# Optimization experiments

Hardware: AMD Instinct MI355X
Metric: run time of the kernel (lower is better)

The kernel has to match this reference:

```python
import jax, jax.numpy as jnp
import numpy as np

EPS = 0.0001
N, E, DIN, H, DH, C, G = 50000, 800000, 256, 4, 64, 10, 100


def setup_inputs() -> dict:
    key = jax.random.key(0)
    ks = jax.random.split(key, 10)
    x = jax.random.normal(ks[0], (N, DIN), dtype=jnp.float32)
    src = jax.random.randint(ks[1], (E,), 0, N)
    dst = jax.random.randint(ks[2], (E,), 0, N)
    midx = jnp.stack([src, dst]).astype(jnp.int32)
    batch = jnp.sort(jax.random.randint(ks[3], (N,), 0, G)).astype(jnp.int32)
    W_feat = jax.random.normal(ks[4], (DIN, H * DH), dtype=jnp.float32) / np.sqrt(DIN)
    phi = jax.random.normal(ks[5], (H, 2 * DH, 1), dtype=jnp.float32) / np.sqrt(2 * DH)
    W1 = jax.random.normal(ks[6], (H * DH, DH), dtype=jnp.float32) / np.sqrt(H * DH)
    b1 = jnp.zeros((DH,), jnp.float32)
    W2 = jax.random.normal(ks[7], (DH, C), dtype=jnp.float32) / np.sqrt(DH)
    b2 = jnp.zeros((C,), jnp.float32)
    return {"x": x, "midx": midx, "batch": batch, "W_feat": W_feat,
            "phi": phi, "W1": W1, "b1": b1, "W2": W2, "b2": b2}


def reference(x, midx, batch, W_feat, phi, W1, b1, W2, b2):
    src, dst = midx[0], midx[1]
    # per-head node features [N, H, DH]
    h = (x @ W_feat).reshape(-1, H, DH)
    # concat-then-matmul with phi == sum of two half projections (GAT trick)
    phi_s = phi[:, :DH, 0]   # [H, DH]
    phi_d = phi[:, DH:, 0]   # [H, DH]
    a_s = jnp.einsum('nhd,hd->nh', h, phi_s)  # [N, H]
    a_d = jnp.einsum('nhd,hd->nh', h, phi_d)
    w = jax.nn.sigmoid(jax.nn.leaky_relu(a_s[src] + a_d[dst]))  # [E, H]
    msg = (h[dst] * w[:, :, None]).reshape(src.shape[0], H * DH)  # [E, H*DH]
    agg = jax.ops.segment_sum(msg, src, num_segments=x.shape[0])  # scatter_add
    # MLP head (dropout is identity in eval mode)
    z = jax.nn.leaky_relu(agg @ W1 + b1) @ W2 + b2  # [N, C]
    tmp = jnp.exp(z - jnp.max(z, axis=-1, keepdims=True)) + EPS
    preds = tmp / jnp.sum(tmp, axis=-1, keepdims=True)
    # global mean pool over graphs
    sums = jax.ops.segment_sum(preds, batch, num_segments=G)
    cnts = jax.ops.segment_sum(jnp.ones((batch.shape[0],), preds.dtype), batch, num_segments=G)
    yp = sums / cnts[:, None]
    return jnp.log(yp), preds
```

## Files before the change

kernel.cpp:

```cpp
#include <hip/hip_runtime.h>
#include <hip/hip_bf16.h>
#include <cstdint>

#define NN   50000
#define EE   800000
#define DIN_ 256
#define HD_  256
#define DH_  64
#define NH_  4
#define NC_  10
#define NG_  100
#define EPS_ 1e-4f
#define SLOPE_ 0.01f
#define AROW 40
#define CAP_ 48

typedef unsigned short ushortT;
typedef __attribute__((ext_vector_type(8))) short short8;
typedef __attribute__((ext_vector_type(4))) float f32x4;

__device__ __forceinline__ float leaky(float x) { return x >= 0.f ? x : SLOPE_ * x; }
__device__ __forceinline__ float sigm(float x)  { return 1.f / (1.f + __expf(-x)); }
__device__ __forceinline__ float b2f(ushortT u) { return __uint_as_float(((unsigned)u) << 16); }
__device__ __forceinline__ ushortT f2b(float f) {
    unsigned u = __float_as_uint(f);
    u += 0x7fffu + ((u >> 16) & 1u);
    return (ushortT)(u >> 16);
}

__global__ void setup_kernel(int* cursor,
                             const float* __restrict__ W, ushortT* __restrict__ wt,
                             const float* __restrict__ W1, ushortT* __restrict__ w1t,
                             const int* __restrict__ batch, int* __restrict__ gstart) {
    int i = blockIdx.x * 256 + threadIdx.x;
    if (i < NN) {
        cursor[i] = 0;
        int b = batch[i];
        int bp = (i == 0) ? -1 : batch[i - 1];
        for (int g = bp + 1; g <= b; g++) gstart[g] = i;
        if (i == NN - 1) {
            for (int g = b + 1; g <= NG_; g++) gstart[g] = NN;
        }
    }
    if (i < DIN_ * HD_) {
        int k = i >> 8, n = i & 255;
        wt[n * DIN_ + k] = f2b(W[i]);
    }
    if (i < 256 * 64) {
        int k = i >> 6, o = i & 63;
        w1t[o * 256 + k] = f2b(W1[i]);
    }
}

__global__ __launch_bounds__(256) void gemm_attn(const float* __restrict__ x,
                                                 const ushortT* __restrict__ wt,
                                                 const float* __restrict__ phi,
                                                 ushortT* __restrict__ hbf,
                                                 float* __restrict__ a_s,
                                                 float* __restrict__ a_d) {
    __shared__ ushortT A_lds[128 * AROW];
    __shared__ ushortT B_lds[128 * AROW];
    const int tid  = threadIdx.x;
    const int wave = tid >> 6, lane = tid & 63;
    const int wm = wave >> 1, wn = wave & 1;
    const int row0 = blockIdx.x * 128;
    const int col0 = blockIdx.y * 128;
    const int q = lane >> 4, l16 = lane & 15;

    f32x4 acc[4][4];
#pragma unroll
    for (int i = 0; i < 4; i++)
#pragma unroll
        for (int j = 0; j < 4; j++) acc[i][j] = (f32x4){0.f, 0.f, 0.f, 0.f};

    const int lm  = tid >> 1;
    const int lko = (tid & 1) * 16;

    for (int k0 = 0; k0 < DIN_; k0 += 32) {
        __syncthreads();
        {
            int gr = row0 + lm;
            float4 a0 = make_float4(0.f,0.f,0.f,0.f), a1 = a0, a2 = a0, a3 = a0;
            if (gr < NN) {
                const float4* xp = (const float4*)(x + (size_t)gr * DIN_ + k0 + lko);
                a0 = xp[0]; a1 = xp[1]; a2 = xp[2]; a3 = xp[3];
            }
            ushortT* ap = &A_lds[lm * AROW + lko];
            *(ushort4*)(ap + 0)  = make_ushort4(f2b(a0.x), f2b(a0.y), f2b(a0.z), f2b(a0.w));
            *(ushort4*)(ap + 4)  = make_ushort4(f2b(a1.x), f2b(a1.y), f2b(a1.z), f2b(a1.w));
            *(ushort4*)(ap + 8)  = make_ushort4(f2b(a2.x), f2b(a2.y), f2b(a2.z), f2b(a2.w));
            *(ushort4*)(ap + 12) = make_ushort4(f2b(a3.x), f2b(a3.y), f2b(a3.z), f2b(a3.w));
        }
        {
            const uint4* wp = (const uint4*)(wt + (size_t)(col0 + lm) * DIN_ + k0 + lko);
            uint4 b0 = wp[0], b1 = wp[1];
            *(uint4*)&B_lds[lm * AROW + lko + 0] = b0;
            *(uint4*)&B_lds[lm * AROW + lko + 8] = b1;
        }
        __syncthreads();

        short8 af[4], bf[4];
#pragma unroll
        for (int mi = 0; mi < 4; mi++)
            af[mi] = *(const short8*)&A_lds[(wm * 64 + mi * 16 + l16) * AROW + q * 8];
#pragma unroll
        for (int ni = 0; ni < 4; ni++)
            bf[ni] = *(const short8*)&B_lds[(wn * 64 + ni * 16 + l16) * AROW + q * 8];
#pragma unroll
        for (int mi = 0; mi < 4; mi++)
#pragma unroll
            for (int ni = 0; ni < 4; ni++)
                acc[mi][ni] = __builtin_amdgcn_mfma_f32_16x16x32_bf16(af[mi], bf[ni], acc[mi][ni], 0, 0, 0);
    }

#pragma unroll
    for (int mi = 0; mi < 4; mi++) {
        int rbase = row0 + wm * 64 + mi * 16 + q * 4;
#pragma unroll
        for (int ni = 0; ni < 4; ni++) {
            int c = col0 + wn * 64 + ni * 16 + l16;
#pragma unroll
            for (int r = 0; r < 4; r++) {
                int gr = rbase + r;
                if (gr < NN) hbf[(size_t)gr * HD_ + c] = f2b(acc[mi][ni][r]);
            }
        }
    }

    int head = blockIdx.y * 2 + wn;
    float phs[4], phd[4];
#pragma unroll
    for (int ni = 0; ni < 4; ni++) {
        phs[ni] = phi[head * 128 + ni * 16 + l16];
        phd[ni] = phi[head * 128 + 64 + ni * 16 + l16];
    }
#pragma unroll
    for (int mi = 0; mi < 4; mi++) {
#pragma unroll
        for (int r = 0; r < 4; r++) {
            float ps = acc[mi][0][r] * phs[0] + acc[mi][1][r] * phs[1]
                     + acc[mi][2][r] * phs[2] + acc[mi][3][r] * phs[3];
            float pd = acc[mi][0][r] * phd[0] + acc[mi][1][r] * phd[1]
                     + acc[mi][2][r] * phd[2] + acc[mi][3][r] * phd[3];
#pragma unroll
            for (int o = 1; o < 16; o <<= 1) {
                ps += __shfl_xor(ps, o);
                pd += __shfl_xor(pd, o);
            }
            if (l16 == 0) {
                int gr = row0 + wm * 64 + mi * 16 + q * 4 + r;
                if (gr < NN) {
                    a_s[gr * 4 + head] = ps;
                    a_d[gr * 4 + head] = pd;
                }
            }
        }
    }
}

__global__ void fill_edges(const int* __restrict__ src, const int* __restrict__ dstA,
                           int* __restrict__ cursor,
                           const float* __restrict__ a_s, const float* __restrict__ a_d,
                           uint4* __restrict__ edges) {
    int e = blockIdx.x * 256 + threadIdx.x;
    if (e >= EE) return;
    int s = src[e], d = dstA[e];
    int slot = atomicAdd(&cursor[s], 1);
    if (slot >= CAP_) return;
    float4 as4 = *(const float4*)(a_s + (size_t)s * 4);
    float4 ad4 = *(const float4*)(a_d + (size_t)d * 4);
    unsigned w01 = (unsigned)f2b(sigm(leaky(as4.x + ad4.x)))
                 | ((unsigned)f2b(sigm(leaky(as4.y + ad4.y))) << 16);
    unsigned w23 = (unsigned)f2b(sigm(leaky(as4.z + ad4.z)))
                 | ((unsigned)f2b(sigm(leaky(as4.w + ad4.w))) << 16);
    edges[(size_t)s * CAP_ + slot] = make_uint4((unsigned)d, w01, w23, 0u);
}

__global__ __launch_bounds__(256) void agg_kernel(const ushortT* __restrict__ hbf,
                                                  const int* __restrict__ cursor,
                                                  const uint4* __restrict__ edges,
                                                  ushortT* __restrict__ aggB) {
    int wv = threadIdx.x >> 6, lane = threadIdx.x & 63;
    int n = blockIdx.x * 4 + wv;
    int hsel = lane >> 4;
    int wsh = (hsel & 1) * 16;
    int cnt = cursor[n];
    if (cnt > CAP_) cnt = CAP_;
    int e0 = n * CAP_, e1 = e0 + cnt;
    float4 acc = make_float4(0.f, 0.f, 0.f, 0.f);
    const ushortT* hbase = hbf + (size_t)lane * 4;

    int i = e0;
    while (i + 8 <= e1) {
        uint4 ee[8]; ushort4 hh[8]; float ww[8];
#pragma unroll
        for (int j = 0; j < 8; j++) ee[j] = edges[i + j];
#pragma unroll
        for (int j = 0; j < 8; j++) {
            unsigned pair = (hsel & 2) ? ee[j].z : ee[j].y;
            ww[j] = b2f((ushortT)((pair >> wsh) & 0xffffu));
            hh[j] = *(const ushort4*)(hbase + (size_t)ee[j].x * HD_);
        }
#pragma unroll
        for (int j = 0; j < 8; j++) {
            acc.x += b2f(hh[j].x) * ww[j];
            acc.y += b2f(hh[j].y) * ww[j];
            acc.z += b2f(hh[j].z) * ww[j];
            acc.w += b2f(hh[j].w) * ww[j];
        }
        i += 8;
    }
    while (i + 4 <= e1) {
        uint4 ee[4]; ushort4 hh[4]; float ww[4];
#pragma unroll
        for (int j = 0; j < 4; j++) ee[j] = edges[i + j];
#pragma unroll
        for (int j = 0; j < 4; j++) {
            unsigned pair = (hsel & 2) ? ee[j].z : ee[j].y;
            ww[j] = b2f((ushortT)((pair >> wsh) & 0xffffu));
            hh[j] = *(const ushort4*)(hbase + (size_t)ee[j].x * HD_);
        }
#pragma unroll
        for (int j = 0; j < 4; j++) {
            acc.x += b2f(hh[j].x) * ww[j];
            acc.y += b2f(hh[j].y) * ww[j];
            acc.z += b2f(hh[j].z) * ww[j];
            acc.w += b2f(hh[j].w) * ww[j];
        }
        i += 4;
    }
    for (; i < e1; i++) {
        uint4 e = edges[i];
        unsigned pair = (hsel & 2) ? e.z : e.y;
        float s = b2f((ushortT)((pair >> wsh) & 0xffffu));
        ushort4 hv = *(const ushort4*)(hbase + (size_t)e.x * HD_);
        acc.x += b2f(hv.x) * s; acc.y += b2f(hv.y) * s;
        acc.z += b2f(hv.z) * s; acc.w += b2f(hv.w) * s;
    }
    ushort4 o4 = make_ushort4(f2b(acc.x), f2b(acc.y), f2b(acc.z), f2b(acc.w));
    *(ushort4*)(aggB + (size_t)n * HD_ + lane * 4) = o4;
}

__global__ __launch_bounds__(256) void mlp_kernel(const ushortT* __restrict__ aggB,
                                                  const ushortT* __restrict__ w1t,
                                                  const float* __restrict__ b1,
                                                  const float* __restrict__ W2,
                                                  const float* __restrict__ b2,
                                                  float* __restrict__ out) {
    __shared__ float z1t[64][65];
    const int tid = threadIdx.x;
    const int wave = tid >> 6, lane = tid & 63;
    const int q = lane >> 4, l16 = lane & 15;
    const int n0 = blockIdx.x * 64;
    const int nodeRow = n0 + wave * 16 + l16;

    f32x4 acc[4];
#pragma unroll
    for (int ni = 0; ni < 4; ni++) acc[ni] = (f32x4){0.f, 0.f, 0.f, 0.f};

    const ushortT* arow = aggB + (size_t)nodeRow * HD_ + q * 8;
#pragma unroll
    for (int k0 = 0; k0 < 256; k0 += 32) {
        short8 af = *(const short8*)(arow + k0);
#pragma unroll
        for (int ni = 0; ni < 4; ni++) {
            short8 bf = *(const short8*)(w1t + (size_t)(ni * 16 + l16) * 256 + k0 + q * 8);
            acc[ni] = __builtin_amdgcn_mfma_f32_16x16x32_bf16(af, bf, acc[ni], 0, 0, 0);
        }
    }
#pragma unroll
    for (int ni = 0; ni < 4; ni++) {
        int o = ni * 16 + l16;
        float bb = b1[o];
#pragma unroll
        for (int r = 0; r < 4; r++)
            z1t[o][wave * 16 + q * 4 + r] = leaky(acc[ni][r] + bb);
    }
    __syncthreads();

    if (tid < 64) {
        int n = n0 + tid;
        if (n < NN) {
            float zc[NC_];
#pragma unroll
            for (int c = 0; c < NC_; c++) zc[c] = b2[c];
            for (int k = 0; k < 64; k++) {
                float zv = z1t[k][tid];
#pragma unroll
                for (int c = 0; c < NC_; c++) zc[c] += zv * W2[k * NC_ + c];
            }
            float m = zc[0];
#pragma unroll
            for (int c = 1; c < NC_; c++) m = fmaxf(m, zc[c]);
            float ssum = 0.f;
#pragma unroll
            for (int c = 0; c < NC_; c++) { zc[c] = __expf(zc[c] - m) + EPS_; ssum += zc[c]; }
            float inv = 1.f / ssum;
#pragma unroll
            for (int c = 0; c < NC_; c++) out[1000 + (size_t)n * NC_ + c] = zc[c] * inv;
        }
    }
}

__global__ __launch_bounds__(256) void group_mean(const float* __restrict__ preds,
                                                  const int* __restrict__ gstart,
                                                  float* __restrict__ out) {
    __shared__ float red[16][16];
    int g = blockIdx.x;
    int t = threadIdx.x;
    int c = t & 15, chunk = t >> 4;
    int gs = gstart[g], ge = gstart[g + 1];
    float s = 0.f;
    if (c < NC_) {
        for (int n = gs + chunk; n < ge; n += 16) s += preds[(size_t)n * NC_ + c];
    }
    red[chunk][c] = s;
    __syncthreads();
    if (t < NC_) {
        float tot = 0.f;
#pragma unroll
        for (int j = 0; j < 16; j++) tot += red[j][t];
        out[g * NC_ + t] = __logf(tot / (float)(ge - gs));
    }
}

extern "C" void kernel_launch(void* const* d_in, const int* in_sizes, int n_in,
                              void* d_out, int out_size, void* d_ws, size_t ws_size,
                              hipStream_t stream) {
    const float* x      = (const float*)d_in[0];
    const int*   midx   = (const int*)d_in[1];
    const int*   batch  = (const int*)d_in[2];
    const float* W_feat = (const float*)d_in[3];
    const float* phi    = (const float*)d_in[4];
    const float* W1     = (const float*)d_in[5];
    const float* b1     = (const float*)d_in[6];
    const float* W2     = (const float*)d_in[7];
    const float* b2     = (const float*)d_in[8];
    const int* src = midx;
    const int* dst = midx + EE;
    float* out = (float*)d_out;

    char* p = (char*)d_ws;
    auto alloc = [&](size_t bytes) { void* r = (void*)p; p += (bytes + 255) & ~(size_t)255; return r; };
    ushortT* hbf      = (ushortT*)alloc((size_t)NN * HD_ * 2);
    ushortT* aggB     = (ushortT*)alloc((size_t)NN * HD_ * 2);
    uint4*   edges    = (uint4*)alloc((size_t)NN * CAP_ * 16);
    ushortT* wt       = (ushortT*)alloc((size_t)DIN_ * HD_ * 2);
    ushortT* w1t      = (ushortT*)alloc((size_t)64 * 256 * 2);
    float*   a_s      = (float*)alloc((size_t)NN * 4 * 4);
    float*   a_d      = (float*)alloc((size_t)NN * 4 * 4);
    int*     cursor   = (int*)alloc((size_t)NN * 4);
    int*     gstart   = (int*)alloc((size_t)(NG_ + 1) * 4);

    setup_kernel<<<256, 256, 0, stream>>>(cursor, W_feat, wt, W1, w1t, batch, gstart);
    gemm_attn<<<dim3((NN + 127) / 128, 2), 256, 0, stream>>>(x, wt, phi, hbf, a_s, a_d);
    fill_edges<<<(EE + 255) / 256, 256, 0, stream>>>(src, dst, cursor, a_s, a_d, edges);
    agg_kernel<<<NN / 4, 256, 0, stream>>>(hbf, cursor, edges, aggB);
    mlp_kernel<<<(NN + 63) / 64, 256, 0, stream>>>(aggB, w1t, b1, W2, b2, out);
    group_mean<<<NG_, 256, 0, stream>>>(out + 1000, gstart, out);
}
```

Baseline: 265.7 us.

## Fuse edge aggregation and MLP head into one kernel via LDS staging

Merges the aggregation kernel and the MLP kernel so each block aggregates 16 nodes into shared memory and immediately runs the W1 MFMA, the W2 projection and the softmax on them. This removes the global round trip of the 50000x256 bf16 aggregate buffer and one kernel launch. In exchange each block now processes 16 nodes with each wave doing four nodes sequentially, and only 16 threads run the tail MLP, so there is less parallelism per block and more serialized latency in the gather loop.

```diff
diff --git a/kernel.cpp b/kernel.cpp
--- a/kernel.cpp
+++ b/kernel.cpp
@@ -14,6 +14,7 @@
 #define SLOPE_ 0.01f
 #define AROW 40
 #define CAP_ 48
+#define FROW 264
 
 typedef unsigned short ushortT;
 typedef __attribute__((ext_vector_type(8))) short short8;
@@ -176,129 +177,124 @@
     edges[(size_t)s * CAP_ + slot] = make_uint4((unsigned)d, w01, w23, 0u);
 }
 
-__global__ __launch_bounds__(256) void agg_kernel(const ushortT* __restrict__ hbf,
-                                                  const int* __restrict__ cursor,
-                                                  const uint4* __restrict__ edges,
-                                                  ushortT* __restrict__ aggB) {
-    int wv = threadIdx.x >> 6, lane = threadIdx.x & 63;
-    int n = blockIdx.x * 4 + wv;
-    int hsel = lane >> 4;
-    int wsh = (hsel & 1) * 16;
-    int cnt = cursor[n];
-    if (cnt > CAP_) cnt = CAP_;
-    int e0 = n * CAP_, e1 = e0 + cnt;
-    float4 acc = make_float4(0.f, 0.f, 0.f, 0.f);
-    const ushortT* hbase = hbf + (size_t)lane * 4;
-
-    int i = e0;
-    while (i + 8 <= e1) {
-        uint4 ee[8]; ushort4 hh[8]; float ww[8];
-#pragma unroll
-        for (int j = 0; j < 8; j++) ee[j] = edges[i + j];
-#pragma unroll
-        for (int j = 0; j < 8; j++) {
-            unsigned pair = (hsel & 2) ? ee[j].z : ee[j].y;
-            ww[j] = b2f((ushortT)((pair >> wsh) & 0xffffu));
-            hh[j] = *(const ushort4*)(hbase + (size_t)ee[j].x * HD_);
-        }
-#pragma unroll
-        for (int j = 0; j < 8; j++) {
-            acc.x += b2f(hh[j].x) * ww[j];
-            acc.y += b2f(hh[j].y) * ww[j];
-            acc.z += b2f(hh[j].z) * ww[j];
-            acc.w += b2f(hh[j].w) * ww[j];
-        }
-        i += 8;
-    }
-    while (i + 4 <= e1) {
-        uint4 ee[4]; ushort4 hh[4]; float ww[4];
-#pragma unroll
-        for (int j = 0; j < 4; j++) ee[j] = edges[i + j];
-#pragma unroll
-        for (int j = 0; j < 4; j++) {
-            unsigned pair = (hsel & 2) ? ee[j].z : ee[j].y;
-            ww[j] = b2f((ushortT)((pair >> wsh) & 0xffffu));
-            hh[j] = *(const ushort4*)(hbase + (size_t)ee[j].x * HD_);
-        }
-#pragma unroll
-        for (int j = 0; j < 4; j++) {
-            acc.x += b2f(hh[j].x) * ww[j];
-            acc.y += b2f(hh[j].y) * ww[j];
-            acc.z += b2f(hh[j].z) * ww[j];
-            acc.w += b2f(hh[j].w) * ww[j];
-        }
-        i += 4;
-    }
-    for (; i < e1; i++) {
-        uint4 e = edges[i];
-        unsigned pair = (hsel & 2) ? e.z : e.y;
-        float s = b2f((ushortT)((pair >> wsh) & 0xffffu));
-        ushort4 hv = *(const ushort4*)(hbase + (size_t)e.x * HD_);
-        acc.x += b2f(hv.x) * s; acc.y += b2f(hv.y) * s;
-        acc.z += b2f(hv.z) * s; acc.w += b2f(hv.w) * s;
-    }
-    ushort4 o4 = make_ushort4(f2b(acc.x), f2b(acc.y), f2b(acc.z), f2b(acc.w));
-    *(ushort4*)(aggB + (size_t)n * HD_ + lane * 4) = o4;
-}
-
-__global__ __launch_bounds__(256) void mlp_kernel(const ushortT* __restrict__ aggB,
-                                                  const ushortT* __restrict__ w1t,
-                                                  const float* __restrict__ b1,
-                                                  const float* __restrict__ W2,
-                                                  const float* __restrict__ b2,
-                                                  float* __restrict__ out) {
-    __shared__ float z1t[64][65];
+__global__ __launch_bounds__(256) void agg_mlp(const ushortT* __restrict__ hbf,
+                                               const int* __restrict__ cursor,
+                                               const uint4* __restrict__ edges,
+                                               const ushortT* __restrict__ w1t,
+                                               const float* __restrict__ b1,
+                                               const float* __restrict__ W2,
+                                               const float* __restrict__ b2,
+                                               float* __restrict__ out) {
+    __shared__ ushortT A_lds[16 * FROW];
+    __shared__ float z1t[16][68];
     const int tid = threadIdx.x;
     const int wave = tid >> 6, lane = tid & 63;
     const int q = lane >> 4, l16 = lane & 15;
-    const int n0 = blockIdx.x * 64;
-    const int nodeRow = n0 + wave * 16 + l16;
-
-    f32x4 acc[4];
-#pragma unroll
-    for (int ni = 0; ni < 4; ni++) acc[ni] = (f32x4){0.f, 0.f, 0.f, 0.f};
-
-    const ushortT* arow = aggB + (size_t)nodeRow * HD_ + q * 8;
+    const int hsel = lane >> 4;
+    const int wsh = (hsel & 1) * 16;
+    const int n0 = blockIdx.x * 16;
+    const ushortT* hbase = hbf + (size_t)lane * 4;
+
+#pragma unroll
+    for (int ii = 0; ii < 4; ii++) {
+        int ln = wave * 4 + ii;
+        int n = n0 + ln;
+        int cnt = cursor[n];
+        if (cnt > CAP_) cnt = CAP_;
+        int e0 = n * CAP_, e1 = e0 + cnt;
+        float4 acc = make_float4(0.f, 0.f, 0.f, 0.f);
+
+        int i = e0;
+        while (i + 8 <= e1) {
+            uint4 ee[8]; ushort4 hh[8]; float ww[8];
+#pragma unroll
+            for (int j = 0; j < 8; j++) ee[j] = edges[i + j];
+#pragma unroll
+            for (int j = 0; j < 8; j++) {
+                unsigned pair = (hsel & 2) ? ee[j].z : ee[j].y;
+                ww[j] = b2f((ushortT)((pair >> wsh) & 0xffffu));
+                hh[j] = *(const ushort4*)(hbase + (size_t)ee[j].x * HD_);
+            }
+#pragma unroll
+            for (int j = 0; j < 8; j++) {
+                acc.x += b2f(hh[j].x) * ww[j];
+                acc.y += b2f(hh[j].y) * ww[j];
+                acc.z += b2f(hh[j].z) * ww[j];
+                acc.w += b2f(hh[j].w) * ww[j];
+            }
+            i += 8;
+        }
+        while (i + 4 <= e1) {
+            uint4 ee[4]; ushort4 hh[4]; float ww[4];
+#pragma unroll
+            for (int j = 0; j < 4; j++) ee[j] = edges[i + j];
+#pragma unroll
+            for (int j = 0; j < 4; j++) {
+                unsigned pair = (hsel & 2) ? ee[j].z : ee[j].y;
+                ww[j] = b2f((ushortT)((pair >> wsh) & 0xffffu));
+                hh[j] = *(const ushort4*)(hbase + (size_t)ee[j].x * HD_);
+            }
+#pragma unroll
+            for (int j = 0; j < 4; j++) {
+                acc.x += b2f(hh[j].x) * ww[j];
+                acc.y += b2f(hh[j].y) * ww[j];
+                acc.z += b2f(hh[j].z) * ww[j];
+                acc.w += b2f(hh[j].w) * ww[j];
+            }
+            i += 4;
+        }
+        for (; i < e1; i++) {
+            uint4 e = edges[i];
+            unsigned pair = (hsel & 2) ? e.z : e.y;
+            float s = b2f((ushortT)((pair >> wsh) & 0xffffu));
+            ushort4 hv = *(const ushort4*)(hbase + (size_t)e.x * HD_);
+            acc.x += b2f(hv.x) * s; acc.y += b2f(hv.y) * s;
+            acc.z += b2f(hv.z) * s; acc.w += b2f(hv.w) * s;
+        }
+        ushort4 o4 = make_ushort4(f2b(acc.x), f2b(acc.y), f2b(acc.z), f2b(acc.w));
+        *(ushort4*)&A_lds[ln * FROW + lane * 4] = o4;
+    }
+    __syncthreads();
+
+    f32x4 macc = (f32x4){0.f, 0.f, 0.f, 0.f};
 #pragma unroll
     for (int k0 = 0; k0 < 256; k0 += 32) {
-        short8 af = *(const short8*)(arow + k0);
-#pragma unroll
-        for (int ni = 0; ni < 4; ni++) {
-            short8 bf = *(const short8*)(w1t + (size_t)(ni * 16 + l16) * 256 + k0 + q * 8);
-            acc[ni] = __builtin_amdgcn_mfma_f32_16x16x32_bf16(af, bf, acc[ni], 0, 0, 0);
-        }
-    }
-#pragma unroll
-    for (int ni = 0; ni < 4; ni++) {
-        int o = ni * 16 + l16;
+        short8 af = *(const short8*)&A_lds[l16 * FROW + k0 + q * 8];
+        short8 bf = *(const short8*)(w1t + (size_t)(wave * 16 + l16) * 256 + k0 + q * 8);
+        macc = __builtin_amdgcn_mfma_f32_16x16x32_bf16(af, bf, macc, 0, 0, 0);
+    }
+    {
+        int o = wave * 16 + l16;
         float bb = b1[o];
 #pragma unroll
         for (int r = 0; r < 4; r++)
-            z1t[o][wave * 16 + q * 4 + r] = leaky(acc[ni][r] + bb);
+            z1t[q * 4 + r][o] = leaky(macc[r] + bb);
     }
     __syncthreads();
 
-    if (tid < 64) {
+    if (tid < 16) {
         int n = n0 + tid;
-        if (n < NN) {
-            float zc[NC_];
-#pragma unroll
-            for (int c = 0; c < NC_; c++) zc[c] = b2[c];
-            for (int k = 0; k < 64; k++) {
-                float zv = z1t[k][tid];
-#pragma unroll
-                for (int c = 0; c < NC_; c++) zc[c] += zv * W2[k * NC_ + c];
-            }
-            float m = zc[0];
-#pragma unroll
-            for (int c = 1; c < NC_; c++) m = fmaxf(m, zc[c]);
-            float ssum = 0.f;
-#pragma unroll
-            for (int c = 0; c < NC_; c++) { zc[c] = __expf(zc[c] - m) + EPS_; ssum += zc[c]; }
-            float inv = 1.f / ssum;
-#pragma unroll
-            for (int c = 0; c < NC_; c++) out[1000 + (size_t)n * NC_ + c] = zc[c] * inv;
-        }
+        float zc[NC_];
+#pragma unroll
+        for (int c = 0; c < NC_; c++) zc[c] = b2[c];
+        for (int k = 0; k < 64; k += 4) {
+            float4 z4 = *(const float4*)&z1t[tid][k];
+#pragma unroll
+            for (int j = 0; j < 4; j++) {
+                float zv = (j == 0) ? z4.x : (j == 1) ? z4.y : (j == 2) ? z4.z : z4.w;
+#pragma unroll
+                for (int c = 0; c < NC_; c++) zc[c] += zv * W2[(k + j) * NC_ + c];
+            }
+        }
+        float m = zc[0];
+#pragma unroll
+        for (int c = 1; c < NC_; c++) m = fmaxf(m, zc[c]);
+        float ssum = 0.f;
+#pragma unroll
+        for (int c = 0; c < NC_; c++) { zc[c] = __expf(zc[c] - m) + EPS_; ssum += zc[c]; }
+        float inv = 1.f / ssum;
+#pragma unroll
+        for (int c = 0; c < NC_; c++) out[1000 + (size_t)n * NC_ + c] = zc[c] * inv;
     }
 }
 
@@ -343,7 +339,6 @@
     char* p = (char*)d_ws;
     auto alloc = [&](size_t bytes) { void* r = (void*)p; p += (bytes + 255) & ~(size_t)255; return r; };
     ushortT* hbf      = (ushortT*)alloc((size_t)NN * HD_ * 2);
-    ushortT* aggB     = (ushortT*)alloc((size_t)NN * HD_ * 2);
     uint4*   edges    = (uint4*)alloc((size_t)NN * CAP_ * 16);
     ushortT* wt       = (ushortT*)alloc((size_t)DIN_ * HD_ * 2);
     ushortT* w1t      = (ushortT*)alloc((size_t)64 * 256 * 2);
@@ -355,7 +350,6 @@
     setup_kernel<<<256, 256, 0, stream>>>(cursor, W_feat, wt, W1, w1t, batch, gstart);
     gemm_attn<<<dim3((NN + 127) / 128, 2), 256, 0, stream>>>(x, wt, phi, hbf, a_s, a_d);
     fill_edges<<<(EE + 255) / 256, 256, 0, stream>>>(src, dst, cursor, a_s, a_d, edges);
-    agg_kernel<<<NN / 4, 256, 0, stream>>>(hbf, cursor, edges, aggB);
-    mlp_kernel<<<(NN + 63) / 64, 256, 0, stream>>>(aggB, w1t, b1, W2, b2, out);
+    agg_mlp<<<NN / 16, 256, 0, stream>>>(hbf, cursor, edges, w1t, b1, W2, b2, out);
     group_mean<<<NG_, 256, 0, stream>>>(out + 1000, gstart, out);
 }
```

New measurement: 256.1 us. 1.04x faster.
